# Kernel tuning notes

Hardware: AMD Instinct MI355X
Metric: run time of the kernel (lower is better)

Reference implementation:

```python
import jax, jax.numpy as jnp
import numpy as np

N_NODES = 100000
N_EDGES = 600000
HIDDEN = 128
LN_EPS = 1e-8


def setup_inputs() -> dict:
    key = jax.random.key(0)
    k1, k2, k3 = jax.random.split(key, 3)
    x = jax.random.normal(k1, (N_NODES, HIDDEN), dtype=jnp.float32)
    edge_index = jax.random.randint(k2, (2, N_EDGES), 0, N_NODES, dtype=jnp.int32)
    # GCNConv linear weight (glorot-ish scale) and bias
    W = jax.random.normal(k3, (HIDDEN, HIDDEN), dtype=jnp.float32) / np.sqrt(HIDDEN)
    b = jnp.zeros((HIDDEN,), dtype=jnp.float32)
    ln_gamma = jnp.ones((HIDDEN,), dtype=jnp.float32)
    ln_beta = jnp.zeros((HIDDEN,), dtype=jnp.float32)
    return {"x": x, "edge_index": edge_index, "W": W, "b": b,
            "ln_gamma": ln_gamma, "ln_beta": ln_beta}


def _gcn_layer(x, edge_index, W, b, ln_gamma, ln_beta):
    n = x.shape[0]
    # --- GCNConv (PyG semantics): add self-loops, sym-normalize, x@W, scatter ---
    loop = jnp.arange(n, dtype=edge_index.dtype)
    src = jnp.concatenate([edge_index[0], loop])  # [E+N]
    dst = jnp.concatenate([edge_index[1], loop])
    deg = jax.ops.segment_sum(jnp.ones_like(dst, dtype=x.dtype), dst,
                              num_segments=n)  # in-degree incl. self-loop
    dinv = jnp.where(deg > 0, jax.lax.rsqrt(deg), 0.0)
    norm = dinv[src] * dinv[dst]  # [E+N]
    h = x @ W  # [N, H]
    msg = h[src] * norm[:, None]  # gather + scale, [E+N, H]
    agg = jax.ops.segment_sum(msg, dst, num_segments=n) + b  # scatter-sum
    # --- ReLU -> (dropout = identity in eval) -> residual -> LayerNorm ---
    y = jax.nn.relu(agg) + x
    mu = jnp.mean(y, axis=-1, keepdims=True)
    var = jnp.mean(jnp.square(y - mu), axis=-1, keepdims=True)
    return (y - mu) * jax.lax.rsqrt(var + LN_EPS) * ln_gamma + ln_beta


def reference(x, edge_index, W, b, ln_gamma, ln_beta):
    return _gcn_layer(x, edge_index, W, b, ln_gamma, ln_beta)
```

## Files before the change

kernel.cpp:

```cpp
#include <hip/hip_runtime.h>

#define HID 128
#define CAP 32
#define BM 64
#define EUN 8

typedef unsigned short u16;
typedef unsigned int u32;
typedef __attribute__((ext_vector_type(8))) short short8v;
typedef __attribute__((ext_vector_type(2))) float f32x2;
typedef __attribute__((ext_vector_type(4))) float f32x4;
typedef __attribute__((ext_vector_type(4))) u32 u32x4;

__device__ inline u16 f2bf(float f) {
    union { float f; u32 u; } c; c.f = f;
    u32 u = c.u;
    return (u16)((u + 0x7FFFu + ((u >> 16) & 1u)) >> 16);
}
__device__ inline u32 pack2(float lo, float hi) {
    return (u32)f2bf(lo) | ((u32)f2bf(hi) << 16);
}
__device__ inline float bflo(u32 u) {
    union { u32 u; float f; } c; c.u = u << 16; return c.f;
}
__device__ inline float bfhi(u32 u) {
    union { u32 u; float f; } c; c.u = u & 0xFFFF0000u; return c.f;
}
__device__ inline float bf2f(u16 b) {
    union { u32 u; float f; } c; c.u = ((u32)b) << 16; return c.f;
}

__global__ __launch_bounds__(256) void k_countfill(const int* __restrict__ src,
                                                   const int* __restrict__ dst,
                                                   int* __restrict__ cnt,
                                                   int* __restrict__ csr, int e) {
    const int base = blockIdx.x * (256 * EUN) + threadIdx.x;
    int d[EUN], s[EUN], slot[EUN];
    #pragma unroll
    for (int u = 0; u < EUN; ++u) {
        int i = base + u * 256;
        if (i < e) {
            d[u] = __builtin_nontemporal_load(&dst[i]);
            s[u] = __builtin_nontemporal_load(&src[i]);
        }
    }
    #pragma unroll
    for (int u = 0; u < EUN; ++u)
        if (base + u * 256 < e) slot[u] = atomicAdd(&cnt[d[u]], 1);
    #pragma unroll
    for (int u = 0; u < EUN; ++u)
        if (base + u * 256 < e && slot[u] < CAP)
            csr[(size_t)d[u] * CAP + slot[u]] = s[u];
}

__global__ __launch_bounds__(256) void k_prep(const float* __restrict__ x,
                                              u16* __restrict__ xbf,
                                              u32* __restrict__ x8,
                                              const int* __restrict__ cnt,
                                              const float* __restrict__ W,
                                              u16* __restrict__ wswz, int n) {
    int t = blockIdx.x * blockDim.x + threadIdx.x;
    if (t < n * 16) {
        int g = t >> 4, l = t & 15;
        const float4* p = (const float4*)&x[(size_t)g * HID + l * 8];
        float4 v0 = p[0], v1 = p[1];
        uint4 o;
        o.x = pack2(v0.x, v0.y);
        o.y = pack2(v0.z, v0.w);
        o.z = pack2(v1.x, v1.y);
        o.w = pack2(v1.z, v1.w);
        *(uint4*)&xbf[(size_t)g * HID + l * 8] = o;
        float dd = rsqrtf((float)(cnt[g] + 1));
        u32 a = (u32)__builtin_amdgcn_cvt_pk_fp8_f32(v0.x * dd, v0.y * dd, 0, false);
        a = (u32)__builtin_amdgcn_cvt_pk_fp8_f32(v0.z * dd, v0.w * dd, a, true);
        u32 bq = (u32)__builtin_amdgcn_cvt_pk_fp8_f32(v1.x * dd, v1.y * dd, 0, false);
        bq = (u32)__builtin_amdgcn_cvt_pk_fp8_f32(v1.z * dd, v1.w * dd, bq, true);
        *(uint2*)&x8[(size_t)g * 32 + l * 2] = make_uint2(a, bq);
    }
    if (t < 128 * 128) {
        int i = t & 7;
        int lane = (t >> 3) & 63;
        int ct = (t >> 9) & 7;
        int ks = t >> 12;
        int k = ks * 32 + (lane >> 4) * 8 + i;
        int col = ct * 16 + (lane & 15);
        wswz[t] = f2bf(W[k * HID + col]);
    }
}

__global__ __launch_bounds__(256) void k_fused(const u16* __restrict__ xbf,
                                               const u32* __restrict__ x8,
                                               const int* __restrict__ cnt,
                                               const int* __restrict__ csr,
                                               const u16* __restrict__ wswz,
                                               const float* __restrict__ bvec,
                                               const float* __restrict__ gamma,
                                               const float* __restrict__ beta,
                                               float* __restrict__ out, int n) {
    __shared__ uint4 lds4[1024];
    char* lds = (char*)lds4;
    const int tid = threadIdx.x;
    const int row0 = blockIdx.x * BM;

    {
        const int grp = tid >> 4;
        const int l16 = tid & 15;
        const int j8 = l16 * 8;
        #pragma unroll
        for (int k = 0; k < 4; ++k) {
            int r = grp * 4 + k;
            int g = row0 + r;
            uint4 pk = make_uint4(0, 0, 0, 0);
            if (g < n) {
                const int len = min(cnt[g], CAP);
                const float dd = rsqrtf((float)(cnt[g] + 1));
                float sum[8] = {0.f, 0.f, 0.f, 0.f, 0.f, 0.f, 0.f, 0.f};
                const size_t off = (size_t)g * CAP;
                for (int base = 0; base < len; base += 16) {
                    int idx = base + l16;
                    int sk = (idx < len) ? csr[off + idx] : n;
                    int mm = (min(16, len - base) + 3) & ~3;
                    for (int j = 0; j < mm; j += 4) {
                        int s0 = __shfl(sk, j + 0, 16);
                        int s1 = __shfl(sk, j + 1, 16);
                        int s2 = __shfl(sk, j + 2, 16);
                        int s3 = __shfl(sk, j + 3, 16);
                        uint2 h0 = *(const uint2*)&x8[(size_t)s0 * 32 + l16 * 2];
                        uint2 h1 = *(const uint2*)&x8[(size_t)s1 * 32 + l16 * 2];
                        uint2 h2 = *(const uint2*)&x8[(size_t)s2 * 32 + l16 * 2];
                        uint2 h3 = *(const uint2*)&x8[(size_t)s3 * 32 + l16 * 2];
                        f32x2 p0, p1, p2, p3;
                        p0 = __builtin_amdgcn_cvt_pk_f32_fp8(h0.x, false);
                        p1 = __builtin_amdgcn_cvt_pk_f32_fp8(h0.x, true);
                        p2 = __builtin_amdgcn_cvt_pk_f32_fp8(h0.y, false);
                        p3 = __builtin_amdgcn_cvt_pk_f32_fp8(h0.y, true);
                        sum[0] += p0.x; sum[1] += p0.y; sum[2] += p1.x; sum[3] += p1.y;
                        sum[4] += p2.x; sum[5] += p2.y; sum[6] += p3.x; sum[7] += p3.y;
                        p0 = __builtin_amdgcn_cvt_pk_f32_fp8(h1.x, false);
                        p1 = __builtin_amdgcn_cvt_pk_f32_fp8(h1.x, true);
                        p2 = __builtin_amdgcn_cvt_pk_f32_fp8(h1.y, false);
                        p3 = __builtin_amdgcn_cvt_pk_f32_fp8(h1.y, true);
                        sum[0] += p0.x; sum[1] += p0.y; sum[2] += p1.x; sum[3] += p1.y;
                        sum[4] += p2.x; sum[5] += p2.y; sum[6] += p3.x; sum[7] += p3.y;
                        p0 = __builtin_amdgcn_cvt_pk_f32_fp8(h2.x, false);
                        p1 = __builtin_amdgcn_cvt_pk_f32_fp8(h2.x, true);
                        p2 = __builtin_amdgcn_cvt_pk_f32_fp8(h2.y, false);
                        p3 = __builtin_amdgcn_cvt_pk_f32_fp8(h2.y, true);
                        sum[0] += p0.x; sum[1] += p0.y; sum[2] += p1.x; sum[3] += p1.y;
                        sum[4] += p2.x; sum[5] += p2.y; sum[6] += p3.x; sum[7] += p3.y;
                        p0 = __builtin_amdgcn_cvt_pk_f32_fp8(h3.x, false);
                        p1 = __builtin_amdgcn_cvt_pk_f32_fp8(h3.x, true);
                        p2 = __builtin_amdgcn_cvt_pk_f32_fp8(h3.y, false);
                        p3 = __builtin_amdgcn_cvt_pk_f32_fp8(h3.y, true);
                        sum[0] += p0.x; sum[1] += p0.y; sum[2] += p1.x; sum[3] += p1.y;
                        sum[4] += p2.x; sum[5] += p2.y; sum[6] += p3.x; sum[7] += p3.y;
                    }
                }
                float dd2 = dd * dd;
                u32x4 hv = *(const u32x4*)&xbf[(size_t)g * HID + j8];
                float a0 = fmaf(sum[0], dd, bflo(hv.x) * dd2);
                float a1 = fmaf(sum[1], dd, bfhi(hv.x) * dd2);
                float a2 = fmaf(sum[2], dd, bflo(hv.y) * dd2);
                float a3 = fmaf(sum[3], dd, bfhi(hv.y) * dd2);
                float a4 = fmaf(sum[4], dd, bflo(hv.z) * dd2);
                float a5 = fmaf(sum[5], dd, bfhi(hv.z) * dd2);
                float a6 = fmaf(sum[6], dd, bflo(hv.w) * dd2);
                float a7 = fmaf(sum[7], dd, bfhi(hv.w) * dd2);
                pk.x = pack2(a0, a1);
                pk.y = pack2(a2, a3);
                pk.z = pack2(a4, a5);
                pk.w = pack2(a6, a7);
            }
            int byte = r * 256 + l16 * 16;
            byte ^= (r & 7) << 4;
            *(uint4*)(lds + byte) = pk;
        }
    }
    __syncthreads();

    const int w = tid >> 6;
    const int l = tid & 63;
    const int c15 = l & 15;
    const short8v* wfrag = (const short8v*)wswz;

    f32x4 acc[8];
    #pragma unroll
    for (int c = 0; c < 8; ++c) acc[c] = (f32x4){0.f, 0.f, 0.f, 0.f};

    #pragma unroll
    for (int ks = 0; ks < 4; ++ks) {
        int row = w * 16 + c15;
        int byte = row * 256 + ks * 64 + (l >> 4) * 16;
        byte ^= (row & 7) << 4;
        short8v a = *(const short8v*)(lds + byte);
        #pragma unroll
        for (int ct = 0; ct < 8; ++ct) {
            short8v b = wfrag[(ks * 8 + ct) * 64 + l];
            acc[ct] = __builtin_amdgcn_mfma_f32_16x16x32_bf16(a, b, acc[ct], 0, 0, 0);
        }
    }

    float bb[8], gg[8], bz[8];
    #pragma unroll
    for (int ct = 0; ct < 8; ++ct) {
        bb[ct] = bvec[ct * 16 + c15];
        gg[ct] = gamma[ct * 16 + c15];
        bz[ct] = beta[ct * 16 + c15];
    }
    #pragma unroll
    for (int j = 0; j < 4; ++j) {
        int gr = row0 + w * 16 + (l >> 4) * 4 + j;
        if (gr < n) {
            const u16* xr = xbf + (size_t)gr * HID + c15;
            float v[8];
            #pragma unroll
            for (int ct = 0; ct < 8; ++ct)
                v[ct] = fmaxf(acc[ct][j] + bb[ct], 0.f) + bf2f(xr[ct * 16]);
            float sum = 0.f;
            #pragma unroll
            for (int ct = 0; ct < 8; ++ct) sum += v[ct];
            #pragma unroll
            for (int o = 1; o < 16; o <<= 1) sum += __shfl_xor(sum, o, 16);
            float mu = sum * (1.0f / HID);
            float d[8], vs = 0.f;
            #pragma unroll
            for (int ct = 0; ct < 8; ++ct) { d[ct] = v[ct] - mu; vs = fmaf(d[ct], d[ct], vs); }
            #pragma unroll
            for (int o = 1; o < 16; o <<= 1) vs += __shfl_xor(vs, o, 16);
            float inv = rsqrtf(vs * (1.0f / HID) + 1e-8f);
            float* orow = out + (size_t)gr * HID + c15;
            #pragma unroll
            for (int ct = 0; ct < 8; ++ct)
                __builtin_nontemporal_store(fmaf(d[ct] * inv, gg[ct], bz[ct]), &orow[ct * 16]);
        }
    }
}

extern "C" void kernel_launch(void* const* d_in, const int* in_sizes, int n_in,
                              void* d_out, int out_size, void* d_ws, size_t ws_size,
                              hipStream_t stream) {
    const float* x     = (const float*)d_in[0];
    const int*   ei    = (const int*)d_in[1];
    const float* W     = (const float*)d_in[2];
    const float* b     = (const float*)d_in[3];
    const float* gamma = (const float*)d_in[4];
    const float* beta  = (const float*)d_in[5];
    float* out = (float*)d_out;

    const int n = in_sizes[0] / HID;
    const int e = in_sizes[1] / 2;
    const int* src = ei;
    const int* dst = ei + e;

    u16* xbf  = (u16*)d_ws;
    u32* x8   = (u32*)(xbf + (size_t)n * HID);
    int* cnt  = (int*)(x8 + ((size_t)n + 1) * 32);
    int* csr  = cnt + n;
    u16* wswz = (u16*)(csr + (size_t)n * CAP);

    hipMemsetAsync(x8 + (size_t)n * 32, 0, 128 + (size_t)n * sizeof(int), stream);
    k_countfill<<<(e + 256 * EUN - 1) / (256 * EUN), 256, 0, stream>>>(src, dst, cnt, csr, e);
    k_prep<<<((size_t)n * 16 + 255) / 256, 256, 0, stream>>>(x, xbf, x8, cnt, W, wswz, n);
    k_fused<<<(n + BM - 1) / BM, 256, 0, stream>>>(
        xbf, x8, cnt, csr, wswz, b, gamma, beta, out, n);
}
```

Baseline: 96.91 us.

## Interleave neighbor gathers across four rows to raise memory-level parallelism

The aggregation loop now processes the four rows each 16-lane group owns together. It first loads counts and the first 16 CSR indices for all four rows, then issues fp8 gathers for the rows in round-robin so more independent loads are in flight. Rows with more than 16 neighbors finish their tail separately. This costs more registers, with 32 accumulators held per thread, and adds divergence when rows have different lengths, which may lower occupancy.

```diff
diff --git a/kernel.cpp b/kernel.cpp
--- a/kernel.cpp
+++ b/kernel.cpp
@@ -88,6 +88,43 @@
     }
 }
 
+__device__ inline void gather4(const u32* __restrict__ x8, int sk, int j, int l16,
+                               float* __restrict__ sums) {
+    int s0 = __shfl(sk, j + 0, 16);
+    int s1 = __shfl(sk, j + 1, 16);
+    int s2 = __shfl(sk, j + 2, 16);
+    int s3 = __shfl(sk, j + 3, 16);
+    uint2 h0 = *(const uint2*)&x8[(size_t)s0 * 32 + l16 * 2];
+    uint2 h1 = *(const uint2*)&x8[(size_t)s1 * 32 + l16 * 2];
+    uint2 h2 = *(const uint2*)&x8[(size_t)s2 * 32 + l16 * 2];
+    uint2 h3 = *(const uint2*)&x8[(size_t)s3 * 32 + l16 * 2];
+    f32x2 p0, p1, p2, p3;
+    p0 = __builtin_amdgcn_cvt_pk_f32_fp8(h0.x, false);
+    p1 = __builtin_amdgcn_cvt_pk_f32_fp8(h0.x, true);
+    p2 = __builtin_amdgcn_cvt_pk_f32_fp8(h0.y, false);
+    p3 = __builtin_amdgcn_cvt_pk_f32_fp8(h0.y, true);
+    sums[0] += p0.x; sums[1] += p0.y; sums[2] += p1.x; sums[3] += p1.y;
+    sums[4] += p2.x; sums[5] += p2.y; sums[6] += p3.x; sums[7] += p3.y;
+    p0 = __builtin_amdgcn_cvt_pk_f32_fp8(h1.x, false);
+    p1 = __builtin_amdgcn_cvt_pk_f32_fp8(h1.x, true);
+    p2 = __builtin_amdgcn_cvt_pk_f32_fp8(h1.y, false);
+    p3 = __builtin_amdgcn_cvt_pk_f32_fp8(h1.y, true);
+    sums[0] += p0.x; sums[1] += p0.y; sums[2] += p1.x; sums[3] += p1.y;
+    sums[4] += p2.x; sums[5] += p2.y; sums[6] += p3.x; sums[7] += p3.y;
+    p0 = __builtin_amdgcn_cvt_pk_f32_fp8(h2.x, false);
+    p1 = __builtin_amdgcn_cvt_pk_f32_fp8(h2.x, true);
+    p2 = __builtin_amdgcn_cvt_pk_f32_fp8(h2.y, false);
+    p3 = __builtin_amdgcn_cvt_pk_f32_fp8(h2.y, true);
+    sums[0] += p0.x; sums[1] += p0.y; sums[2] += p1.x; sums[3] += p1.y;
+    sums[4] += p2.x; sums[5] += p2.y; sums[6] += p3.x; sums[7] += p3.y;
+    p0 = __builtin_amdgcn_cvt_pk_f32_fp8(h3.x, false);
+    p1 = __builtin_amdgcn_cvt_pk_f32_fp8(h3.x, true);
+    p2 = __builtin_amdgcn_cvt_pk_f32_fp8(h3.y, false);
+    p3 = __builtin_amdgcn_cvt_pk_f32_fp8(h3.y, true);
+    sums[0] += p0.x; sums[1] += p0.y; sums[2] += p1.x; sums[3] += p1.y;
+    sums[4] += p2.x; sums[5] += p2.y; sums[6] += p3.x; sums[7] += p3.y;
+}
+
 __global__ __launch_bounds__(256) void k_fused(const u16* __restrict__ xbf,
                                                const u32* __restrict__ x8,
                                                const int* __restrict__ cnt,
@@ -106,71 +143,61 @@
         const int grp = tid >> 4;
         const int l16 = tid & 15;
         const int j8 = l16 * 8;
+
+        float sums[4][8] = {};
+        int gN[4], lenN[4], skN[4], mmN[4];
+        float ddN[4];
         #pragma unroll
         for (int k = 0; k < 4; ++k) {
-            int r = grp * 4 + k;
-            int g = row0 + r;
+            int g = row0 + grp * 4 + k;
+            gN[k] = g;
+            int c = (g < n) ? cnt[g] : 0;
+            lenN[k] = min(c, CAP);
+            ddN[k] = rsqrtf((float)(c + 1));
+            skN[k] = (g < n && l16 < lenN[k]) ? csr[(size_t)g * CAP + l16] : n;
+            mmN[k] = (min(16, lenN[k]) + 3) & ~3;
+        }
+        int mmax = max(max(mmN[0], mmN[1]), max(mmN[2], mmN[3]));
+
+        for (int j = 0; j < mmax; j += 4) {
+            #pragma unroll
+            for (int k = 0; k < 4; ++k)
+                if (j < mmN[k]) gather4(x8, skN[k], j, l16, sums[k]);
+        }
+
+        #pragma unroll
+        for (int k = 0; k < 4; ++k) {
+            if (lenN[k] > 16) {
+                const size_t off = (size_t)gN[k] * CAP;
+                for (int base = 16; base < lenN[k]; base += 16) {
+                    int idx = base + l16;
+                    int sk = (idx < lenN[k]) ? csr[off + idx] : n;
+                    int m4 = (min(16, lenN[k] - base) + 3) & ~3;
+                    for (int j = 0; j < m4; j += 4) gather4(x8, sk, j, l16, sums[k]);
+                }
+            }
+        }
+
+        #pragma unroll
+        for (int k = 0; k < 4; ++k) {
             uint4 pk = make_uint4(0, 0, 0, 0);
-            if (g < n) {
-                const int len = min(cnt[g], CAP);
-                const float dd = rsqrtf((float)(cnt[g] + 1));
-                float sum[8] = {0.f, 0.f, 0.f, 0.f, 0.f, 0.f, 0.f, 0.f};
-                const size_t off = (size_t)g * CAP;
-                for (int base = 0; base < len; base += 16) {
-                    int idx = base + l16;
-                    int sk = (idx < len) ? csr[off + idx] : n;
-                    int mm = (min(16, len - base) + 3) & ~3;
-                    for (int j = 0; j < mm; j += 4) {
-                        int s0 = __shfl(sk, j + 0, 16);
-                        int s1 = __shfl(sk, j + 1, 16);
-                        int s2 = __shfl(sk, j + 2, 16);
-                        int s3 = __shfl(sk, j + 3, 16);
-                        uint2 h0 = *(const uint2*)&x8[(size_t)s0 * 32 + l16 * 2];
-                        uint2 h1 = *(const uint2*)&x8[(size_t)s1 * 32 + l16 * 2];
-                        uint2 h2 = *(const uint2*)&x8[(size_t)s2 * 32 + l16 * 2];
-                        uint2 h3 = *(const uint2*)&x8[(size_t)s3 * 32 + l16 * 2];
-                        f32x2 p0, p1, p2, p3;
-                        p0 = __builtin_amdgcn_cvt_pk_f32_fp8(h0.x, false);
-                        p1 = __builtin_amdgcn_cvt_pk_f32_fp8(h0.x, true);
-                        p2 = __builtin_amdgcn_cvt_pk_f32_fp8(h0.y, false);
-                        p3 = __builtin_amdgcn_cvt_pk_f32_fp8(h0.y, true);
-                        sum[0] += p0.x; sum[1] += p0.y; sum[2] += p1.x; sum[3] += p1.y;
-                        sum[4] += p2.x; sum[5] += p2.y; sum[6] += p3.x; sum[7] += p3.y;
-                        p0 = __builtin_amdgcn_cvt_pk_f32_fp8(h1.x, false);
-                        p1 = __builtin_amdgcn_cvt_pk_f32_fp8(h1.x, true);
-                        p2 = __builtin_amdgcn_cvt_pk_f32_fp8(h1.y, false);
-                        p3 = __builtin_amdgcn_cvt_pk_f32_fp8(h1.y, true);
-                        sum[0] += p0.x; sum[1] += p0.y; sum[2] += p1.x; sum[3] += p1.y;
-                        sum[4] += p2.x; sum[5] += p2.y; sum[6] += p3.x; sum[7] += p3.y;
-                        p0 = __builtin_amdgcn_cvt_pk_f32_fp8(h2.x, false);
-                        p1 = __builtin_amdgcn_cvt_pk_f32_fp8(h2.x, true);
-                        p2 = __builtin_amdgcn_cvt_pk_f32_fp8(h2.y, false);
-                        p3 = __builtin_amdgcn_cvt_pk_f32_fp8(h2.y, true);
-                        sum[0] += p0.x; sum[1] += p0.y; sum[2] += p1.x; sum[3] += p1.y;
-                        sum[4] += p2.x; sum[5] += p2.y; sum[6] += p3.x; sum[7] += p3.y;
-                        p0 = __builtin_amdgcn_cvt_pk_f32_fp8(h3.x, false);
-                        p1 = __builtin_amdgcn_cvt_pk_f32_fp8(h3.x, true);
-                        p2 = __builtin_amdgcn_cvt_pk_f32_fp8(h3.y, false);
-                        p3 = __builtin_amdgcn_cvt_pk_f32_fp8(h3.y, true);
-                        sum[0] += p0.x; sum[1] += p0.y; sum[2] += p1.x; sum[3] += p1.y;
-                        sum[4] += p2.x; sum[5] += p2.y; sum[6] += p3.x; sum[7] += p3.y;
-                    }
-                }
-                float dd2 = dd * dd;
-                u32x4 hv = *(const u32x4*)&xbf[(size_t)g * HID + j8];
-                float a0 = fmaf(sum[0], dd, bflo(hv.x) * dd2);
-                float a1 = fmaf(sum[1], dd, bfhi(hv.x) * dd2);
-                float a2 = fmaf(sum[2], dd, bflo(hv.y) * dd2);
-                float a3 = fmaf(sum[3], dd, bfhi(hv.y) * dd2);
-                float a4 = fmaf(sum[4], dd, bflo(hv.z) * dd2);
-                float a5 = fmaf(sum[5], dd, bfhi(hv.z) * dd2);
-                float a6 = fmaf(sum[6], dd, bflo(hv.w) * dd2);
-                float a7 = fmaf(sum[7], dd, bfhi(hv.w) * dd2);
+            if (gN[k] < n) {
+                float dd = ddN[k], dd2 = dd * dd;
+                u32x4 hv = *(const u32x4*)&xbf[(size_t)gN[k] * HID + j8];
+                float a0 = fmaf(sums[k][0], dd, bflo(hv.x) * dd2);
+                float a1 = fmaf(sums[k][1], dd, bfhi(hv.x) * dd2);
+                float a2 = fmaf(sums[k][2], dd, bflo(hv.y) * dd2);
+                float a3 = fmaf(sums[k][3], dd, bfhi(hv.y) * dd2);
+                float a4 = fmaf(sums[k][4], dd, bflo(hv.z) * dd2);
+                float a5 = fmaf(sums[k][5], dd, bfhi(hv.z) * dd2);
+                float a6 = fmaf(sums[k][6], dd, bflo(hv.w) * dd2);
+                float a7 = fmaf(sums[k][7], dd, bfhi(hv.w) * dd2);
                 pk.x = pack2(a0, a1);
                 pk.y = pack2(a2, a3);
                 pk.z = pack2(a4, a5);
                 pk.w = pack2(a6, a7);
             }
+            int r = grp * 4 + k;
             int byte = r * 256 + l16 * 16;
             byte ^= (r & 7) << 4;
             *(uint4*)(lds + byte) = pk;
```

After: 101.2 us. 4.4% more time.
